# Performance work log

Hardware: AMD Instinct MI355X
Metric: run time of the kernel (lower is better)

Reference implementation:

```python
import jax, jax.numpy as jnp
import numpy as np

N_NODES = 100000
N_EDGES = 1600000
NUM_GRAPHS = 128


def setup_inputs() -> dict:
    key = jax.random.key(0)
    k1, k2, k3, k4, k5, k6 = jax.random.split(key, 6)
    x = jax.random.normal(k1, (N_NODES, 69), dtype=jnp.float32)
    src = jax.random.randint(k2, (N_EDGES,), 0, N_NODES)
    dst = jax.random.randint(k3, (N_EDGES,), 0, N_NODES)
    graph_ids = jnp.sort(jax.random.randint(k4, (N_NODES,), 0, NUM_GRAPHS))
    # Glorot-uniform weights like dgl GraphConv (bias=False)
    lim1 = np.sqrt(6.0 / (69 + 128))
    lim2 = np.sqrt(6.0 / (128 + 64))
    W1 = jax.random.uniform(k5, (69, 128), minval=-lim1, maxval=lim1, dtype=jnp.float32)
    W2 = jax.random.uniform(k6, (128, 64), minval=-lim2, maxval=lim2, dtype=jnp.float32)
    return {"x": x, "W1": W1, "W2": W2, "src": src, "dst": dst, "graph_ids": graph_ids}


def _graph_conv(feat, W, src, dst, inv_sqrt_out, inv_sqrt_in, n_nodes):
    # dgl GraphConv norm='both': D_out^{-1/2} -> SpMM(A) -> D_in^{-1/2} -> W
    h = feat * inv_sqrt_out[:, None]
    agg = jax.ops.segment_sum(h[src], dst, num_segments=n_nodes)  # [N, d]
    agg = agg * inv_sqrt_in[:, None]
    return agg @ W


def reference(x, W1, W2, src, dst, graph_ids):
    n = x.shape[0]
    ones = jnp.ones((src.shape[0],), dtype=x.dtype)
    out_deg = jax.ops.segment_sum(ones, src, num_segments=n)
    in_deg = jax.ops.segment_sum(ones, dst, num_segments=n)
    inv_sqrt_out = jax.lax.rsqrt(jnp.clip(out_deg, 1.0, None))
    inv_sqrt_in = jax.lax.rsqrt(jnp.clip(in_deg, 1.0, None))

    h = _graph_conv(x, W1, src, dst, inv_sqrt_out, inv_sqrt_in, n)
    h = jax.nn.relu(h)
    h = _graph_conv(h, W2, src, dst, inv_sqrt_out, inv_sqrt_in, n)
    h = jax.nn.relu(h)
    # dgl.max_nodes: per-graph max readout -> [num_graphs, 64]
    readout = jax.ops.segment_max(h, graph_ids, num_segments=NUM_GRAPHS)
    return readout
```

## Files before the change

### kernel.cpp

```cpp
#include <hip/hip_runtime.h>

#define N_NODES 100000
#define N_EDGES 1600000
#define NUM_GRAPHS 128

#define BSH 10
#define NBUCK 98
#define NBLKP 500
#define EPB (N_EDGES / NBLKP)
#define SOFF (NBUCK * NBLKP)
#define NSCAN (2 * NBUCK * NBLKP)
#define SCAN_BS 1024
#define NBSC ((NSCAN + SCAN_BS - 1) / SCAN_BS)

__device__ __forceinline__ unsigned bf16pair(float a, float b) {
    unsigned ua = __float_as_uint(a), ub = __float_as_uint(b);
    ua = (ua + 0x7FFFu + ((ua >> 16) & 1u)) >> 16;
    ub = (ub + 0x7FFFu + ((ub >> 16) & 1u)) >> 16;
    return ua | (ub << 16);
}
__device__ __forceinline__ float bflo(unsigned u) { return __uint_as_float(u << 16); }
__device__ __forceinline__ float bfhi(unsigned u) { return __uint_as_float(u & 0xFFFF0000u); }

__global__ __launch_bounds__(256) void part_hist(const int* __restrict__ src,
                                                 const int* __restrict__ dst,
                                                 int* __restrict__ cnt) {
    __shared__ int hd[4 * NBUCK], hs[4 * NBUCK];
    int t = threadIdx.x;
    for (int i = t; i < 4 * NBUCK; i += 256) { hd[i] = 0; hs[i] = 0; }
    __syncthreads();
    int wid = t >> 6;
    int* hdw = hd + wid * NBUCK;
    int* hsw = hs + wid * NBUCK;
    int e0 = blockIdx.x * EPB;
    for (int j = 4 * t; j + 3 < EPB; j += 1024) {
        int4 s4 = *(const int4*)(src + e0 + j);
        int4 d4 = *(const int4*)(dst + e0 + j);
        atomicAdd(&hdw[d4.x >> BSH], 1); atomicAdd(&hdw[d4.y >> BSH], 1);
        atomicAdd(&hdw[d4.z >> BSH], 1); atomicAdd(&hdw[d4.w >> BSH], 1);
        atomicAdd(&hsw[s4.x >> BSH], 1); atomicAdd(&hsw[s4.y >> BSH], 1);
        atomicAdd(&hsw[s4.z >> BSH], 1); atomicAdd(&hsw[s4.w >> BSH], 1);
    }
    __syncthreads();
    int bk = blockIdx.x;
    for (int i = t; i < NBUCK; i += 256) {
        cnt[i * NBLKP + bk] = hd[i] + hd[NBUCK + i] + hd[2 * NBUCK + i] + hd[3 * NBUCK + i];
        cnt[SOFF + i * NBLKP + bk] = hs[i] + hs[NBUCK + i] + hs[2 * NBUCK + i] + hs[3 * NBUCK + i];
    }
}

__global__ __launch_bounds__(256) void scan1(const int* __restrict__ cnt, int* __restrict__ excl,
                                             int* __restrict__ blksum, int n) {
    __shared__ int tmp[256];
    int t = threadIdx.x;
    int idx0 = blockIdx.x * SCAN_BS + t * 4;
    int v[4];
#pragma unroll
    for (int k = 0; k < 4; ++k) { int i = idx0 + k; v[k] = (i < n) ? cnt[i] : 0; }
    int sum = v[0] + v[1] + v[2] + v[3];
    tmp[t] = sum;
    __syncthreads();
    for (int off = 1; off < 256; off <<= 1) {
        int y = (t >= off) ? tmp[t - off] : 0;
        __syncthreads();
        tmp[t] += y;
        __syncthreads();
    }
    int run = (t > 0) ? tmp[t - 1] : 0;
#pragma unroll
    for (int k = 0; k < 4; ++k) { int i = idx0 + k; if (i < n) excl[i] = run; run += v[k]; }
    if (t == 255) blksum[blockIdx.x] = tmp[255];
}

__global__ __launch_bounds__(256) void scan2(int* __restrict__ blksum, int nb) {
    __shared__ int tmp[256];
    int t = threadIdx.x;
    int C = (nb + 255) / 256;
    int base = t * C;
    int s = 0;
    for (int k = 0; k < C; ++k) { int i = base + k; if (i < nb) s += blksum[i]; }
    tmp[t] = s;
    __syncthreads();
    for (int off = 1; off < 256; off <<= 1) {
        int y = (t >= off) ? tmp[t - off] : 0;
        __syncthreads();
        tmp[t] += y;
        __syncthreads();
    }
    int run = (t > 0) ? tmp[t - 1] : 0;
    for (int k = 0; k < C; ++k) {
        int i = base + k;
        if (i < nb) { int v = blksum[i]; blksum[i] = run; run += v; }
    }
}

__global__ __launch_bounds__(256) void part_scatter(const int* __restrict__ src,
                                                    const int* __restrict__ dst,
                                                    const int* __restrict__ cnt,
                                                    const int* __restrict__ blk,
                                                    unsigned* __restrict__ pdst,
                                                    unsigned short* __restrict__ psrc) {
    __shared__ int cd[NBUCK], cs[NBUCK];
    int bk = blockIdx.x;
    int t = threadIdx.x;
    for (int i = t; i < NBUCK; i += 256) {
        int ii = i * NBLKP + bk;
        cd[i] = cnt[ii] + blk[ii >> 10];
        int jj = SOFF + i * NBLKP + bk;
        cs[i] = cnt[jj] + blk[jj >> 10] - N_EDGES;
    }
    __syncthreads();
    int e0 = bk * EPB;
    for (int j = 4 * t; j + 3 < EPB; j += 1024) {
        int4 s4 = *(const int4*)(src + e0 + j);
        int4 d4 = *(const int4*)(dst + e0 + j);
        int ss[4] = { s4.x, s4.y, s4.z, s4.w };
        int dd[4] = { d4.x, d4.y, d4.z, d4.w };
#pragma unroll
        for (int u = 0; u < 4; ++u) {
            int s = ss[u], d = dd[u];
            int pd = atomicAdd(&cd[d >> BSH], 1);
            pdst[pd] = (unsigned)s | ((unsigned)(d & 1023) << 17);
            int ps = atomicAdd(&cs[s >> BSH], 1);
            psrc[ps] = (unsigned short)(s & 1023);
        }
    }
}

__global__ __launch_bounds__(1024) void phase_d(const unsigned* __restrict__ pdst,
                                                const unsigned short* __restrict__ psrc,
                                                const int* __restrict__ cnt,
                                                const int* __restrict__ blk,
                                                int* __restrict__ ecol, int* __restrict__ row_start,
                                                float* __restrict__ isqi, float* __restrict__ isqo,
                                                const float* __restrict__ x,
                                                unsigned* __restrict__ xsu,
                                                int nN) {
    __shared__ int lh[1024];
    __shared__ int lsc[1024];
    __shared__ float scs[1024];
    int t = threadIdx.x;
    if (blockIdx.x < NBUCK) {
        int bu = blockIdx.x;
        int i0 = bu * NBLKP;
        int b0 = cnt[i0] + blk[i0 >> 10];
        int b1;
        if (bu == NBUCK - 1) b1 = N_EDGES;
        else { int i1 = i0 + NBLKP; b1 = cnt[i1] + blk[i1 >> 10]; }
        lh[t] = 0;
        __syncthreads();
        for (int j = b0 + t; j < b1; j += 1024)
            atomicAdd(&lh[pdst[j] >> 17], 1);
        __syncthreads();
        int myc = lh[t];
        lsc[t] = myc;
        __syncthreads();
        for (int off = 1; off < 1024; off <<= 1) {
            int y = (t >= off) ? lsc[t - off] : 0;
            __syncthreads();
            lsc[t] += y;
            __syncthreads();
        }
        int excl = lsc[t] - myc;
        int node = (bu << BSH) + t;
        if (node < nN) {
            row_start[node] = b0 + excl;
            isqi[node] = rsqrtf(fmaxf((float)myc, 1.0f));
        }
        __syncthreads();
        lh[t] = b0 + excl;
        __syncthreads();
        for (int j = b0 + t; j < b1; j += 1024) {
            unsigned w = pdst[j];
            int pos = atomicAdd(&lh[w >> 17], 1);
            ecol[pos] = (int)(w & 0x1FFFFu);
        }
    } else {
        int bu = blockIdx.x - NBUCK;
        int i0 = SOFF + bu * NBLKP;
        int b0 = cnt[i0] + blk[i0 >> 10] - N_EDGES;
        int b1;
        if (bu == NBUCK - 1) b1 = N_EDGES;
        else { int i1 = i0 + NBLKP; b1 = cnt[i1] + blk[i1 >> 10] - N_EDGES; }
        lh[t] = 0;
        __syncthreads();
        for (int j = b0 + t; j < b1; j += 1024)
            atomicAdd(&lh[psrc[j]], 1);
        __syncthreads();
        int n0 = bu << BSH;
        float v = rsqrtf(fmaxf((float)lh[t], 1.0f));
        scs[t] = v;
        int node = n0 + t;
        if (node < nN) isqo[node] = v;
        __syncthreads();
        int rows = min(1024, nN - n0);
        if (rows <= 0) return;
        for (int idx = t; idx < rows * 36; idx += 1024) {
            int r = idx / 36, c2 = idx - r * 36;
            float s = scs[r];
            int c = 2 * c2;
            float a = (c < 69) ? x[(size_t)(n0 + r) * 69 + c] * s : 0.0f;
            float b = (c + 1 < 69) ? x[(size_t)(n0 + r) * 69 + c + 1] * s : 0.0f;
            xsu[(size_t)(n0 + r) * 36 + c2] = bf16pair(a, b);
        }
    }
}

__global__ void gather1_kernel(const unsigned* __restrict__ feat, const int* __restrict__ ecol,
                               const int* __restrict__ row_start, const float* __restrict__ dscale,
                               float* __restrict__ agg, int nN, int nE) {
    int wave = (int)(((unsigned)blockIdx.x * blockDim.x + threadIdx.x) >> 6);
    int lane = threadIdx.x & 63;
    if (wave >= nN) return;
    int beg = row_start[wave];
    int end = (wave == nN - 1) ? nE : row_start[wave + 1];
    bool act = (lane < 36);
    float ax = 0.0f, ay = 0.0f;
    for (int j0 = beg; j0 < end; j0 += 64) {
        int ne = min(64, end - j0);
        int eidx = (lane < ne) ? ecol[j0 + lane] : 0;
        int k = 0;
        for (; k + 8 <= ne; k += 8) {
            unsigned v[8];
#pragma unroll
            for (int u = 0; u < 8; ++u) {
                int s = __shfl(eidx, k + u);
                v[u] = act ? feat[(size_t)s * 36 + lane] : 0u;
            }
#pragma unroll
            for (int u = 0; u < 8; ++u) { ax += bflo(v[u]); ay += bfhi(v[u]); }
        }
        for (; k + 2 <= ne; k += 2) {
            int s0 = __shfl(eidx, k), s1 = __shfl(eidx, k + 1);
            unsigned v0 = act ? feat[(size_t)s0 * 36 + lane] : 0u;
            unsigned v1 = act ? feat[(size_t)s1 * 36 + lane] : 0u;
            ax += bflo(v0) + bflo(v1); ay += bfhi(v0) + bfhi(v1);
        }
        for (; k < ne; ++k) {
            int s = __shfl(eidx, k);
            unsigned v = act ? feat[(size_t)s * 36 + lane] : 0u;
            ax += bflo(v); ay += bfhi(v);
        }
    }
    if (act) {
        float dsc = dscale[wave];
        ((float2*)(agg + (size_t)wave * 72))[lane] = make_float2(ax * dsc, ay * dsc);
    }
}

__global__ void gather2_kernel(const unsigned* __restrict__ feat, const int* __restrict__ ecol,
                               const int* __restrict__ row_start, const float* __restrict__ dscale,
                               float* __restrict__ agg, int nN, int nE) {
    int wave = (int)(((unsigned)blockIdx.x * blockDim.x + threadIdx.x) >> 6);
    int lane = threadIdx.x & 63;
    if (wave >= nN) return;
    int beg = row_start[wave];
    int end = (wave == nN - 1) ? nE : row_start[wave + 1];
    int half = lane >> 5;
    int c = lane & 31;
    float ax = 0.0f, ay = 0.0f;
    for (int j0 = beg; j0 < end; j0 += 64) {
        int ne = min(64, end - j0);
        int eidx = (lane < ne) ? ecol[j0 + lane] : 0;
        int k = 0;
        for (; k + 16 <= ne; k += 16) {
            unsigned v[8];
#pragma unroll
            for (int u = 0; u < 8; ++u) {
                int s = __shfl(eidx, k + 2 * u + half);
                v[u] = feat[(size_t)s * 32 + c];
            }
#pragma unroll
            for (int u = 0; u < 8; ++u) { ax += bflo(v[u]); ay += bfhi(v[u]); }
        }
        for (; k + 2 <= ne; k += 2) {
            int s = __shfl(eidx, k + half);
            unsigned v = feat[(size_t)s * 32 + c];
            ax += bflo(v); ay += bfhi(v);
        }
        if (k < ne) {
            int s = __shfl(eidx, k);
            if (half == 0) {
                unsigned v = feat[(size_t)s * 32 + c];
                ax += bflo(v); ay += bfhi(v);
            }
        }
    }
    ax += __shfl_xor(ax, 32);
    ay += __shfl_xor(ay, 32);
    if (half == 0) {
        float dsc = dscale[wave];
        ((float2*)(agg + (size_t)wave * 64))[c] = make_float2(ax * dsc, ay * dsc);
    }
}

template<int KP, int K, int NO, bool RELU, bool SCALE, bool BF16OUT, bool BF16IN>
__global__ __launch_bounds__(256) void node_gemm(const void* __restrict__ in,
                                                 const float* __restrict__ W,
                                                 const float* __restrict__ rowscale,
                                                 void* __restrict__ out, int nN) {
    constexpr int CG = NO / 8;
    constexpr int RT = 256 / CG;
    constexpr int ROWS = RT * 4;
    __shared__ float Wl[KP * NO];
    for (int i = threadIdx.x; i < KP * NO; i += 256)
        Wl[i] = (i < K * NO) ? W[i] : 0.0f;
    __syncthreads();

    int cg = threadIdx.x % CG;
    int rt = threadIdx.x / CG;
    int row0 = blockIdx.x * ROWS + rt * 4;
    int c0 = cg * 8;

    float4 accL[4] = {};
    float4 accH[4] = {};
    int rclamp[4];
#pragma unroll
    for (int r = 0; r < 4; ++r) rclamp[r] = min(row0 + r, nN - 1);

    if (BF16IN) {
        const unsigned* inu = (const unsigned*)in;
#pragma unroll 2
        for (int k8 = 0; k8 < KP / 8; ++k8) {
            uint4 a4[4];
#pragma unroll
            for (int r = 0; r < 4; ++r)
                a4[r] = *(const uint4*)(inu + (size_t)rclamp[r] * (KP / 2) + k8 * 4);
#pragma unroll
            for (int kk = 0; kk < 8; ++kk) {
                int k = k8 * 8 + kk;
                float4 wlo = *(const float4*)&Wl[k * NO + c0];
                float4 whi = *(const float4*)&Wl[k * NO + c0 + 4];
#pragma unroll
                for (int r = 0; r < 4; ++r) {
                    unsigned wd = ((const unsigned*)&a4[r])[kk >> 1];
                    float ar = (kk & 1) ? bfhi(wd) : bflo(wd);
                    accL[r].x += ar * wlo.x; accL[r].y += ar * wlo.y;
                    accL[r].z += ar * wlo.z; accL[r].w += ar * wlo.w;
                    accH[r].x += ar * whi.x; accH[r].y += ar * whi.y;
                    accH[r].z += ar * whi.z; accH[r].w += ar * whi.w;
                }
            }
        }
    } else {
        const float* inf = (const float*)in;
#pragma unroll 2
        for (int k4 = 0; k4 < KP / 4; ++k4) {
            float4 a[4];
#pragma unroll
            for (int r = 0; r < 4; ++r)
                a[r] = *(const float4*)(inf + (size_t)rclamp[r] * KP + k4 * 4);
#pragma unroll
            for (int kk = 0; kk < 4; ++kk) {
                int k = k4 * 4 + kk;
                float4 wlo = *(const float4*)&Wl[k * NO + c0];
                float4 whi = *(const float4*)&Wl[k * NO + c0 + 4];
#pragma unroll
                for (int r = 0; r < 4; ++r) {
                    float ar = (kk == 0) ? a[r].x : (kk == 1) ? a[r].y : (kk == 2) ? a[r].z : a[r].w;
                    accL[r].x += ar * wlo.x; accL[r].y += ar * wlo.y;
                    accL[r].z += ar * wlo.z; accL[r].w += ar * wlo.w;
                    accH[r].x += ar * whi.x; accH[r].y += ar * whi.y;
                    accH[r].z += ar * whi.z; accH[r].w += ar * whi.w;
                }
            }
        }
    }

#pragma unroll
    for (int r = 0; r < 4; ++r) {
        int row = row0 + r;
        if (row < nN) {
            float4 lo = accL[r], hi = accH[r];
            if (SCALE) {
                float sc = rowscale[row];
                lo.x *= sc; lo.y *= sc; lo.z *= sc; lo.w *= sc;
                hi.x *= sc; hi.y *= sc; hi.z *= sc; hi.w *= sc;
            }
            if (RELU) {
                lo.x = fmaxf(lo.x, 0.f); lo.y = fmaxf(lo.y, 0.f);
                lo.z = fmaxf(lo.z, 0.f); lo.w = fmaxf(lo.w, 0.f);
                hi.x = fmaxf(hi.x, 0.f); hi.y = fmaxf(hi.y, 0.f);
                hi.z = fmaxf(hi.z, 0.f); hi.w = fmaxf(hi.w, 0.f);
            }
            if (BF16OUT) {
                unsigned* ob = (unsigned*)out;
                uint4 p;
                p.x = bf16pair(lo.x, lo.y); p.y = bf16pair(lo.z, lo.w);
                p.z = bf16pair(hi.x, hi.y); p.w = bf16pair(hi.z, hi.w);
                *(uint4*)(ob + (size_t)row * (NO / 2) + c0 / 2) = p;
            } else {
                float* of = (float*)out;
                *(float4*)(of + (size_t)row * NO + c0) = lo;
                *(float4*)(of + (size_t)row * NO + c0 + 4) = hi;
            }
        }
    }
}

__global__ void readout_kernel(const float* __restrict__ agg2, const int* __restrict__ gid,
                               unsigned* __restrict__ out, int nN) {
    const int NPW = 32;
    int wave = (int)(((unsigned)blockIdx.x * blockDim.x + threadIdx.x) >> 6);
    int lane = threadIdx.x & 63;
    int n0 = wave * NPW;
    if (n0 >= nN) return;
    int curg = gid[n0];
    float best = 0.0f;
    for (int i = 0; i < NPW; ++i) {
        int n = n0 + i;
        if (n >= nN) break;
        int g = gid[n];
        float v = fmaxf(agg2[(size_t)n * 64 + lane], 0.0f);
        if (g != curg) {
            atomicMax(&out[curg * 64 + lane], __float_as_uint(best));
            curg = g;
            best = v;
        } else {
            best = fmaxf(best, v);
        }
    }
    atomicMax(&out[curg * 64 + lane], __float_as_uint(best));
}

extern "C" void kernel_launch(void* const* d_in, const int* in_sizes, int n_in,
                              void* d_out, int out_size, void* d_ws, size_t ws_size,
                              hipStream_t stream) {
    const float* x   = (const float*)d_in[0];
    const float* W1  = (const float*)d_in[1];
    const float* W2  = (const float*)d_in[2];
    const int*   src = (const int*)d_in[3];
    const int*   dst = (const int*)d_in[4];
    const int*   gid = (const int*)d_in[5];

    char* w = (char*)d_ws;
    float* isqo    = (float*)w;                 w += N_NODES * 4;
    float* isqi    = (float*)w;                 w += N_NODES * 4;
    int* row_start = (int*)w;                   w += N_NODES * 4;
    int* ecol      = (int*)w;                   w += (size_t)N_EDGES * 4;
    int* cnt       = (int*)w;                   w += (size_t)NSCAN * 4;
    int* blksum    = (int*)w;                   w += 1024 * 4;
    float* bufA    = (float*)w;                 w += (size_t)N_NODES * 72 * 4;
    char* bufB     = w;
    unsigned* pdst       = (unsigned*)bufB;
    unsigned short* psrc = (unsigned short*)(bufB + (size_t)N_EDGES * 4);
    unsigned* xsu        = (unsigned*)(bufB + (size_t)N_EDGES * 6);
    unsigned* h1         = (unsigned*)bufB;
    unsigned* y2s        = (unsigned*)bufA;
    float* agg2          = (float*)bufB;

    hipMemsetAsync(d_out, 0, (size_t)out_size * sizeof(float), stream);

    part_hist<<<NBLKP, 256, 0, stream>>>(src, dst, cnt);
    scan1<<<NBSC, 256, 0, stream>>>(cnt, cnt, blksum, NSCAN);
    scan2<<<1, 256, 0, stream>>>(blksum, NBSC);
    part_scatter<<<NBLKP, 256, 0, stream>>>(src, dst, cnt, blksum, pdst, psrc);
    phase_d<<<2 * NBUCK, 1024, 0, stream>>>(pdst, psrc, cnt, blksum, ecol, row_start,
                                            isqi, isqo, x, xsu, N_NODES);

    gather1_kernel<<<(N_NODES * 64 + 255) / 256, 256, 0, stream>>>(
        xsu, ecol, row_start, isqi, bufA, N_NODES, N_EDGES);
    node_gemm<72, 69, 128, true, false, true, false><<<(N_NODES + 63) / 64, 256, 0, stream>>>(
        (const void*)bufA, W1, nullptr, (void*)h1, N_NODES);

    node_gemm<128, 128, 64, false, true, true, true><<<(N_NODES + 127) / 128, 256, 0, stream>>>(
        (const void*)h1, W2, isqo, (void*)y2s, N_NODES);
    gather2_kernel<<<(N_NODES * 64 + 255) / 256, 256, 0, stream>>>(
        y2s, ecol, row_start, isqi, agg2, N_NODES, N_EDGES);

    readout_kernel<<<((N_NODES + 31) / 32 * 64 + 255) / 256, 256, 0, stream>>>(
        agg2, gid, (unsigned*)d_out, N_NODES);
}
```

Baseline: 264.3 us.

## Fuse second gather with max readout and store first aggregation in bf16

The second-layer gather now writes its ReLU'd rows into shared memory, and one wave per block does the per-graph max readout with atomics. This removes the fp32 agg2 round trip through global memory and one kernel launch. Separately, gather1 now packs its output as bf16 pairs and the first GEMM reads it with its BF16IN path, which halves that intermediate traffic. In exchange, precision is lower before W1, and the 1024-thread blocks each wait at a barrier before a serial 16-row readout.

Result: slower. 272.9 us (+3.3%).

```diff
diff --git a/kernel.cpp b/kernel.cpp
--- a/kernel.cpp
+++ b/kernel.cpp
@@ -208,7 +208,7 @@
 
 __global__ void gather1_kernel(const unsigned* __restrict__ feat, const int* __restrict__ ecol,
                                const int* __restrict__ row_start, const float* __restrict__ dscale,
-                               float* __restrict__ agg, int nN, int nE) {
+                               unsigned* __restrict__ agg, int nN, int nE) {
     int wave = (int)(((unsigned)blockIdx.x * blockDim.x + threadIdx.x) >> 6);
     int lane = threadIdx.x & 63;
     if (wave >= nN) return;
@@ -244,53 +244,81 @@
     }
     if (act) {
         float dsc = dscale[wave];
-        ((float2*)(agg + (size_t)wave * 72))[lane] = make_float2(ax * dsc, ay * dsc);
-    }
-}
-
-__global__ void gather2_kernel(const unsigned* __restrict__ feat, const int* __restrict__ ecol,
-                               const int* __restrict__ row_start, const float* __restrict__ dscale,
-                               float* __restrict__ agg, int nN, int nE) {
-    int wave = (int)(((unsigned)blockIdx.x * blockDim.x + threadIdx.x) >> 6);
+        agg[(size_t)wave * 36 + lane] = bf16pair(ax * dsc, ay * dsc);
+    }
+}
+
+__global__ __launch_bounds__(1024) void gather2_readout(const unsigned* __restrict__ feat,
+                                                        const int* __restrict__ ecol,
+                                                        const int* __restrict__ row_start,
+                                                        const float* __restrict__ dscale,
+                                                        const int* __restrict__ gid,
+                                                        unsigned* __restrict__ out, int nN, int nE) {
+    __shared__ float rows[16][64];
+    __shared__ int gids[16];
+    int wv = threadIdx.x >> 6;
     int lane = threadIdx.x & 63;
-    if (wave >= nN) return;
-    int beg = row_start[wave];
-    int end = (wave == nN - 1) ? nE : row_start[wave + 1];
+    int node = blockIdx.x * 16 + wv;
     int half = lane >> 5;
     int c = lane & 31;
-    float ax = 0.0f, ay = 0.0f;
-    for (int j0 = beg; j0 < end; j0 += 64) {
-        int ne = min(64, end - j0);
-        int eidx = (lane < ne) ? ecol[j0 + lane] : 0;
-        int k = 0;
-        for (; k + 16 <= ne; k += 16) {
-            unsigned v[8];
-#pragma unroll
-            for (int u = 0; u < 8; ++u) {
-                int s = __shfl(eidx, k + 2 * u + half);
-                v[u] = feat[(size_t)s * 32 + c];
-            }
-#pragma unroll
-            for (int u = 0; u < 8; ++u) { ax += bflo(v[u]); ay += bfhi(v[u]); }
-        }
-        for (; k + 2 <= ne; k += 2) {
-            int s = __shfl(eidx, k + half);
-            unsigned v = feat[(size_t)s * 32 + c];
-            ax += bflo(v); ay += bfhi(v);
-        }
-        if (k < ne) {
-            int s = __shfl(eidx, k);
-            if (half == 0) {
+    if (node < nN) {
+        int beg = row_start[node];
+        int end = (node == nN - 1) ? nE : row_start[node + 1];
+        float ax = 0.0f, ay = 0.0f;
+        for (int j0 = beg; j0 < end; j0 += 64) {
+            int ne = min(64, end - j0);
+            int eidx = (lane < ne) ? ecol[j0 + lane] : 0;
+            int k = 0;
+            for (; k + 16 <= ne; k += 16) {
+                unsigned v[8];
+#pragma unroll
+                for (int u = 0; u < 8; ++u) {
+                    int s = __shfl(eidx, k + 2 * u + half);
+                    v[u] = feat[(size_t)s * 32 + c];
+                }
+#pragma unroll
+                for (int u = 0; u < 8; ++u) { ax += bflo(v[u]); ay += bfhi(v[u]); }
+            }
+            for (; k + 2 <= ne; k += 2) {
+                int s = __shfl(eidx, k + half);
                 unsigned v = feat[(size_t)s * 32 + c];
                 ax += bflo(v); ay += bfhi(v);
             }
-        }
-    }
-    ax += __shfl_xor(ax, 32);
-    ay += __shfl_xor(ay, 32);
-    if (half == 0) {
-        float dsc = dscale[wave];
-        ((float2*)(agg + (size_t)wave * 64))[c] = make_float2(ax * dsc, ay * dsc);
+            if (k < ne) {
+                int s = __shfl(eidx, k);
+                if (half == 0) {
+                    unsigned v = feat[(size_t)s * 32 + c];
+                    ax += bflo(v); ay += bfhi(v);
+                }
+            }
+        }
+        ax += __shfl_xor(ax, 32);
+        ay += __shfl_xor(ay, 32);
+        if (half == 0) {
+            float dsc = dscale[node];
+            rows[wv][2 * c]     = fmaxf(ax * dsc, 0.0f);
+            rows[wv][2 * c + 1] = fmaxf(ay * dsc, 0.0f);
+        }
+        if (lane == 0) gids[wv] = gid[node];
+    }
+    __syncthreads();
+    if (threadIdx.x < 64) {
+        int col = threadIdx.x;
+        int nv = min(16, nN - blockIdx.x * 16);
+        int curg = gids[0];
+        float best = rows[0][col];
+        for (int i = 1; i < nv; ++i) {
+            int g = gids[i];
+            float v = rows[i][col];
+            if (g != curg) {
+                atomicMax(&out[curg * 64 + col], __float_as_uint(best));
+                curg = g;
+                best = v;
+            } else {
+                best = fmaxf(best, v);
+            }
+        }
+        atomicMax(&out[curg * 64 + col], __float_as_uint(best));
     }
 }
 
@@ -398,31 +426,6 @@
     }
 }
 
-__global__ void readout_kernel(const float* __restrict__ agg2, const int* __restrict__ gid,
-                               unsigned* __restrict__ out, int nN) {
-    const int NPW = 32;
-    int wave = (int)(((unsigned)blockIdx.x * blockDim.x + threadIdx.x) >> 6);
-    int lane = threadIdx.x & 63;
-    int n0 = wave * NPW;
-    if (n0 >= nN) return;
-    int curg = gid[n0];
-    float best = 0.0f;
-    for (int i = 0; i < NPW; ++i) {
-        int n = n0 + i;
-        if (n >= nN) break;
-        int g = gid[n];
-        float v = fmaxf(agg2[(size_t)n * 64 + lane], 0.0f);
-        if (g != curg) {
-            atomicMax(&out[curg * 64 + lane], __float_as_uint(best));
-            curg = g;
-            best = v;
-        } else {
-            best = fmaxf(best, v);
-        }
-    }
-    atomicMax(&out[curg * 64 + lane], __float_as_uint(best));
-}
-
 extern "C" void kernel_launch(void* const* d_in, const int* in_sizes, int n_in,
                               void* d_out, int out_size, void* d_ws, size_t ws_size,
                               hipStream_t stream) {
@@ -440,14 +443,14 @@
     int* ecol      = (int*)w;                   w += (size_t)N_EDGES * 4;
     int* cnt       = (int*)w;                   w += (size_t)NSCAN * 4;
     int* blksum    = (int*)w;                   w += 1024 * 4;
-    float* bufA    = (float*)w;                 w += (size_t)N_NODES * 72 * 4;
+    char* bufA     = w;                         w += (size_t)N_NODES * 72 * 4;
     char* bufB     = w;
     unsigned* pdst       = (unsigned*)bufB;
     unsigned short* psrc = (unsigned short*)(bufB + (size_t)N_EDGES * 4);
     unsigned* xsu        = (unsigned*)(bufB + (size_t)N_EDGES * 6);
+    unsigned* agg1       = (unsigned*)bufA;
     unsigned* h1         = (unsigned*)bufB;
     unsigned* y2s        = (unsigned*)bufA;
-    float* agg2          = (float*)bufB;
 
     hipMemsetAsync(d_out, 0, (size_t)out_size * sizeof(float), stream);
 
@@ -459,15 +462,12 @@
                                             isqi, isqo, x, xsu, N_NODES);
 
     gather1_kernel<<<(N_NODES * 64 + 255) / 256, 256, 0, stream>>>(
-        xsu, ecol, row_start, isqi, bufA, N_NODES, N_EDGES);
-    node_gemm<72, 69, 128, true, false, true, false><<<(N_NODES + 63) / 64, 256, 0, stream>>>(
-        (const void*)bufA, W1, nullptr, (void*)h1, N_NODES);
+        xsu, ecol, row_start, isqi, agg1, N_NODES, N_EDGES);
+    node_gemm<72, 69, 128, true, false, true, true><<<(N_NODES + 63) / 64, 256, 0, stream>>>(
+        (const void*)agg1, W1, nullptr, (void*)h1, N_NODES);
 
     node_gemm<128, 128, 64, false, true, true, true><<<(N_NODES + 127) / 128, 256, 0, stream>>>(
         (const void*)h1, W2, isqo, (void*)y2s, N_NODES);
-    gather2_kernel<<<(N_NODES * 64 + 255) / 256, 256, 0, stream>>>(
-        y2s, ecol, row_start, isqi, agg2, N_NODES, N_EDGES);
-
-    readout_kernel<<<((N_NODES + 31) / 32 * 64 + 255) / 256, 256, 0, stream>>>(
-        agg2, gid, (unsigned*)d_out, N_NODES);
-}
+    gather2_readout<<<(N_NODES + 15) / 16, 1024, 0, stream>>>(
+        y2s, ecol, row_start, isqi, gid, (unsigned*)d_out, N_NODES, N_EDGES);
+}
```

## Store aggregates in bf16, fuse relu into gather2, merge scans into one kernel

Applied to the files above, without the earlier changes.

Gather1 and gather2 now write their aggregated features as packed bf16 pairs instead of fp32. The first GEMM reads bf16 input, and gather2 applies the ReLU before packing. The readout kernel unpacks the bf16 values and indexes its max atomics per column. Separately, the two-level scan (scan1+scan2) is replaced by a single 1024-thread block that scans all counts in place, which removes the block-sum indirection from the scatter kernels. This cuts intermediate memory traffic and one launch, at the cost of bf16 rounding in the aggregates and a serial single-block scan over about 98K entries.

Result: slower. 437.3 us (+65.5%).

```diff
diff --git a/kernel.cpp b/kernel.cpp
--- a/kernel.cpp
+++ b/kernel.cpp
@@ -10,8 +10,6 @@
 #define EPB (N_EDGES / NBLKP)
 #define SOFF (NBUCK * NBLKP)
 #define NSCAN (2 * NBUCK * NBLKP)
-#define SCAN_BS 1024
-#define NBSC ((NSCAN + SCAN_BS - 1) / SCAN_BS)
 
 __device__ __forceinline__ unsigned bf16pair(float a, float b) {
     unsigned ua = __float_as_uint(a), ub = __float_as_uint(b);
@@ -49,65 +47,39 @@
     }
 }
 
-__global__ __launch_bounds__(256) void scan1(const int* __restrict__ cnt, int* __restrict__ excl,
-                                             int* __restrict__ blksum, int n) {
-    __shared__ int tmp[256];
+__global__ __launch_bounds__(1024) void scan_all(int* __restrict__ cnt, int n) {
+    __shared__ int tmp[1024];
     int t = threadIdx.x;
-    int idx0 = blockIdx.x * SCAN_BS + t * 4;
-    int v[4];
-#pragma unroll
-    for (int k = 0; k < 4; ++k) { int i = idx0 + k; v[k] = (i < n) ? cnt[i] : 0; }
-    int sum = v[0] + v[1] + v[2] + v[3];
-    tmp[t] = sum;
-    __syncthreads();
-    for (int off = 1; off < 256; off <<= 1) {
-        int y = (t >= off) ? tmp[t - off] : 0;
-        __syncthreads();
-        tmp[t] += y;
-        __syncthreads();
-    }
-    int run = (t > 0) ? tmp[t - 1] : 0;
-#pragma unroll
-    for (int k = 0; k < 4; ++k) { int i = idx0 + k; if (i < n) excl[i] = run; run += v[k]; }
-    if (t == 255) blksum[blockIdx.x] = tmp[255];
-}
-
-__global__ __launch_bounds__(256) void scan2(int* __restrict__ blksum, int nb) {
-    __shared__ int tmp[256];
-    int t = threadIdx.x;
-    int C = (nb + 255) / 256;
+    const int C = (n + 1023) / 1024;
     int base = t * C;
     int s = 0;
-    for (int k = 0; k < C; ++k) { int i = base + k; if (i < nb) s += blksum[i]; }
+    for (int k = 0; k < C; ++k) { int i = base + k; if (i < n) s += cnt[i]; }
     tmp[t] = s;
     __syncthreads();
-    for (int off = 1; off < 256; off <<= 1) {
+    for (int off = 1; off < 1024; off <<= 1) {
         int y = (t >= off) ? tmp[t - off] : 0;
         __syncthreads();
         tmp[t] += y;
         __syncthreads();
     }
-    int run = (t > 0) ? tmp[t - 1] : 0;
+    int run = tmp[t] - s;
     for (int k = 0; k < C; ++k) {
         int i = base + k;
-        if (i < nb) { int v = blksum[i]; blksum[i] = run; run += v; }
+        if (i < n) { int v = cnt[i]; cnt[i] = run; run += v; }
     }
 }
 
 __global__ __launch_bounds__(256) void part_scatter(const int* __restrict__ src,
                                                     const int* __restrict__ dst,
                                                     const int* __restrict__ cnt,
-                                                    const int* __restrict__ blk,
                                                     unsigned* __restrict__ pdst,
                                                     unsigned short* __restrict__ psrc) {
     __shared__ int cd[NBUCK], cs[NBUCK];
     int bk = blockIdx.x;
     int t = threadIdx.x;
     for (int i = t; i < NBUCK; i += 256) {
-        int ii = i * NBLKP + bk;
-        cd[i] = cnt[ii] + blk[ii >> 10];
-        int jj = SOFF + i * NBLKP + bk;
-        cs[i] = cnt[jj] + blk[jj >> 10] - N_EDGES;
+        cd[i] = cnt[i * NBLKP + bk];
+        cs[i] = cnt[SOFF + i * NBLKP + bk] - N_EDGES;
     }
     __syncthreads();
     int e0 = bk * EPB;
@@ -130,7 +102,6 @@
 __global__ __launch_bounds__(1024) void phase_d(const unsigned* __restrict__ pdst,
                                                 const unsigned short* __restrict__ psrc,
                                                 const int* __restrict__ cnt,
-                                                const int* __restrict__ blk,
                                                 int* __restrict__ ecol, int* __restrict__ row_start,
                                                 float* __restrict__ isqi, float* __restrict__ isqo,
                                                 const float* __restrict__ x,
@@ -142,11 +113,8 @@
     int t = threadIdx.x;
     if (blockIdx.x < NBUCK) {
         int bu = blockIdx.x;
-        int i0 = bu * NBLKP;
-        int b0 = cnt[i0] + blk[i0 >> 10];
-        int b1;
-        if (bu == NBUCK - 1) b1 = N_EDGES;
-        else { int i1 = i0 + NBLKP; b1 = cnt[i1] + blk[i1 >> 10]; }
+        int b0 = cnt[bu * NBLKP];
+        int b1 = (bu == NBUCK - 1) ? N_EDGES : cnt[(bu + 1) * NBLKP];
         lh[t] = 0;
         __syncthreads();
         for (int j = b0 + t; j < b1; j += 1024)
@@ -177,11 +145,8 @@
         }
     } else {
         int bu = blockIdx.x - NBUCK;
-        int i0 = SOFF + bu * NBLKP;
-        int b0 = cnt[i0] + blk[i0 >> 10] - N_EDGES;
-        int b1;
-        if (bu == NBUCK - 1) b1 = N_EDGES;
-        else { int i1 = i0 + NBLKP; b1 = cnt[i1] + blk[i1 >> 10] - N_EDGES; }
+        int b0 = cnt[SOFF + bu * NBLKP] - N_EDGES;
+        int b1 = (bu == NBUCK - 1) ? N_EDGES : cnt[SOFF + (bu + 1) * NBLKP] - N_EDGES;
         lh[t] = 0;
         __syncthreads();
         for (int j = b0 + t; j < b1; j += 1024)
@@ -208,7 +173,7 @@
 
 __global__ void gather1_kernel(const unsigned* __restrict__ feat, const int* __restrict__ ecol,
                                const int* __restrict__ row_start, const float* __restrict__ dscale,
-                               float* __restrict__ agg, int nN, int nE) {
+                               unsigned* __restrict__ agg, int nN, int nE) {
     int wave = (int)(((unsigned)blockIdx.x * blockDim.x + threadIdx.x) >> 6);
     int lane = threadIdx.x & 63;
     if (wave >= nN) return;
@@ -244,13 +209,13 @@
     }
     if (act) {
         float dsc = dscale[wave];
-        ((float2*)(agg + (size_t)wave * 72))[lane] = make_float2(ax * dsc, ay * dsc);
+        agg[(size_t)wave * 36 + lane] = bf16pair(ax * dsc, ay * dsc);
     }
 }
 
 __global__ void gather2_kernel(const unsigned* __restrict__ feat, const int* __restrict__ ecol,
                                const int* __restrict__ row_start, const float* __restrict__ dscale,
-                               float* __restrict__ agg, int nN, int nE) {
+                               unsigned* __restrict__ agg, int nN, int nE) {
     int wave = (int)(((unsigned)blockIdx.x * blockDim.x + threadIdx.x) >> 6);
     int lane = threadIdx.x & 63;
     if (wave >= nN) return;
@@ -290,7 +255,7 @@
     ay += __shfl_xor(ay, 32);
     if (half == 0) {
         float dsc = dscale[wave];
-        ((float2*)(agg + (size_t)wave * 64))[c] = make_float2(ax * dsc, ay * dsc);
+        agg[(size_t)wave * 32 + c] = bf16pair(fmaxf(ax * dsc, 0.0f), fmaxf(ay * dsc, 0.0f));
     }
 }
 
@@ -398,29 +363,32 @@
     }
 }
 
-__global__ void readout_kernel(const float* __restrict__ agg2, const int* __restrict__ gid,
+__global__ void readout_kernel(const unsigned* __restrict__ agg2, const int* __restrict__ gid,
                                unsigned* __restrict__ out, int nN) {
     const int NPW = 32;
     int wave = (int)(((unsigned)blockIdx.x * blockDim.x + threadIdx.x) >> 6);
     int lane = threadIdx.x & 63;
     int n0 = wave * NPW;
     if (n0 >= nN) return;
+    int half = lane >> 5;
+    int c = lane & 31;
     int curg = gid[n0];
     float best = 0.0f;
     for (int i = 0; i < NPW; ++i) {
         int n = n0 + i;
         if (n >= nN) break;
         int g = gid[n];
-        float v = fmaxf(agg2[(size_t)n * 64 + lane], 0.0f);
+        unsigned u = agg2[(size_t)n * 32 + c];
+        float v = half ? bfhi(u) : bflo(u);
         if (g != curg) {
-            atomicMax(&out[curg * 64 + lane], __float_as_uint(best));
+            atomicMax(&out[curg * 64 + 2 * c + half], __float_as_uint(best));
             curg = g;
             best = v;
         } else {
             best = fmaxf(best, v);
         }
     }
-    atomicMax(&out[curg * 64 + lane], __float_as_uint(best));
+    atomicMax(&out[curg * 64 + 2 * c + half], __float_as_uint(best));
 }
 
 extern "C" void kernel_launch(void* const* d_in, const int* in_sizes, int n_in,
@@ -439,29 +407,28 @@
     int* row_start = (int*)w;                   w += N_NODES * 4;
     int* ecol      = (int*)w;                   w += (size_t)N_EDGES * 4;
     int* cnt       = (int*)w;                   w += (size_t)NSCAN * 4;
-    int* blksum    = (int*)w;                   w += 1024 * 4;
-    float* bufA    = (float*)w;                 w += (size_t)N_NODES * 72 * 4;
+    char* bufA     = w;                         w += (size_t)N_NODES * 72 * 4;
     char* bufB     = w;
     unsigned* pdst       = (unsigned*)bufB;
     unsigned short* psrc = (unsigned short*)(bufB + (size_t)N_EDGES * 4);
     unsigned* xsu        = (unsigned*)(bufB + (size_t)N_EDGES * 6);
+    unsigned* agg1       = (unsigned*)bufA;
     unsigned* h1         = (unsigned*)bufB;
     unsigned* y2s        = (unsigned*)bufA;
-    float* agg2          = (float*)bufB;
+    unsigned* agg2       = (unsigned*)bufB;
 
     hipMemsetAsync(d_out, 0, (size_t)out_size * sizeof(float), stream);
 
     part_hist<<<NBLKP, 256, 0, stream>>>(src, dst, cnt);
-    scan1<<<NBSC, 256, 0, stream>>>(cnt, cnt, blksum, NSCAN);
-    scan2<<<1, 256, 0, stream>>>(blksum, NBSC);
-    part_scatter<<<NBLKP, 256, 0, stream>>>(src, dst, cnt, blksum, pdst, psrc);
-    phase_d<<<2 * NBUCK, 1024, 0, stream>>>(pdst, psrc, cnt, blksum, ecol, row_start,
+    scan_all<<<1, 1024, 0, stream>>>(cnt, NSCAN);
+    part_scatter<<<NBLKP, 256, 0, stream>>>(src, dst, cnt, pdst, psrc);
+    phase_d<<<2 * NBUCK, 1024, 0, stream>>>(pdst, psrc, cnt, ecol, row_start,
                                             isqi, isqo, x, xsu, N_NODES);
 
     gather1_kernel<<<(N_NODES * 64 + 255) / 256, 256, 0, stream>>>(
-        xsu, ecol, row_start, isqi, bufA, N_NODES, N_EDGES);
-    node_gemm<72, 69, 128, true, false, true, false><<<(N_NODES + 63) / 64, 256, 0, stream>>>(
-        (const void*)bufA, W1, nullptr, (void*)h1, N_NODES);
+        xsu, ecol, row_start, isqi, agg1, N_NODES, N_EDGES);
+    node_gemm<72, 69, 128, true, false, true, true><<<(N_NODES + 63) / 64, 256, 0, stream>>>(
+        (const void*)agg1, W1, nullptr, (void*)h1, N_NODES);
 
     node_gemm<128, 128, 64, false, true, true, true><<<(N_NODES + 127) / 128, 256, 0, stream>>>(
         (const void*)h1, W2, isqo, (void*)y2s, N_NODES);
```
